# Kernel optimization log

Measured on AMD Instinct MI355X. Metric: run time of the kernel, lower is better.

The kernel has to match this reference:

```python
import jax, jax.numpy as jnp
import numpy as np

EPS = 1e-12  # TF l2_normalize epsilon


def setup_inputs() -> dict:
    key = jax.random.key(0)
    k1, k2 = jax.random.split(key)
    B, V, F = 32, 200000, 400000
    vertices = jax.random.normal(k1, (B, V, 3), dtype=jnp.float32)
    faces = jax.random.randint(k2, (F, 3), 0, V, dtype=jnp.int32)
    return {"vertices": vertices, "faces": faces}


def reference(vertices, faces):
    # vertices: [B, V, 3], faces: [F, 3]
    # Gather triangle vertices: [B, F, 3(verts), 3(xyz)]
    tri = vertices[:, faces, :]
    v0, v1, v2 = tri[..., 0, :], tri[..., 1, :], tri[..., 2, :]
    e1 = v0 - v1
    e2 = v2 - v1
    face_normals = jnp.cross(e2, e1)  # [B, F, 3], unnormalized
    # Scatter-add face normals onto each of the 3 face vertices
    vertex_normals = jnp.zeros_like(vertices)
    for i in range(3):
        vertex_normals = vertex_normals.at[:, faces[:, i], :].add(face_normals)
    # l2 normalize (TF semantics: x * rsqrt(max(sum(x^2), eps)))
    sq = jnp.sum(vertex_normals * vertex_normals, axis=-1, keepdims=True)
    vertex_normals = vertex_normals * jax.lax.rsqrt(jnp.maximum(sq, EPS))
    return vertex_normals
```

## Files before the change

### kernel.cpp

```cpp
#include <hip/hip_runtime.h>

#define EPS 1e-12f
#define CAP 32
#define CAPU 8

typedef unsigned long long ull;


__global__ void zero_ints(int* __restrict__ p, int n) {
    int i = blockIdx.x * blockDim.x + threadIdx.x;
    if (i < n) p[i] = 0;
}

__global__ __launch_bounds__(1024) void prep_kernel(const float* __restrict__ verts,
                                                    float* __restrict__ vT,
                                                    const int* __restrict__ faces,
                                                    int* __restrict__ cursor,
                                                    ull* __restrict__ ell,
                                                    int V, int fblk, int E) {
    __shared__ float sx[32][33], sy[32][33], sz[32][33];
    int bid = blockIdx.x;
    int q = bid / 6, r = bid - 6 * q;
    bool isfill = (r == 5) && (q < fblk);
    if (isfill) {
        int t = q * 1024 + threadIdx.x;
        if (t >= E) return;
        int f = t / 3;
        int c = t - 3 * f;
        int base = 3 * f;
        int iv = faces[base + c];
        int ia = faces[base + (c == 2 ? 0 : c + 1)];
        int ib = faces[base + (c == 0 ? 2 : c - 1)];
        int s = atomicAdd(&cursor[iv], 1);
        if (s < CAP) {
            ull e = ((ull)(unsigned)ib << 32) | (unsigned)ia;
            ell[(size_t)iv * CAP + s] = e;
        }
    } else {
        int t_id = bid - min(q + (r == 5 ? 1 : 0), fblk);
        int tx = threadIdx.x & 31, ty = threadIdx.x >> 5;
        int v0 = t_id * 32;
        const float* p = verts + ((size_t)ty * V + (v0 + tx)) * 3;
        sx[ty][tx] = __builtin_nontemporal_load(p + 0);
        sy[ty][tx] = __builtin_nontemporal_load(p + 1);
        sz[ty][tx] = __builtin_nontemporal_load(p + 2);
        __syncthreads();
        float* o = vT + (size_t)(v0 + ty) * 96;
        o[tx]      = sx[tx][ty];
        o[32 + tx] = sy[tx][ty];
        o[64 + tx] = sz[tx][ty];
    }
}

__global__ __launch_bounds__(1024) void gather_t(const float* __restrict__ vT,
                                                 const int* __restrict__ deg,
                                                 const ull* __restrict__ ell,
                                                 float* __restrict__ out,
                                                 int V) {
    __shared__ float sx[32][33], sy[32][33], sz[32][33];
    int b = threadIdx.x & 31;
    int vi = threadIdx.x >> 5;
    int v = blockIdx.x * 32 + vi;

    int d = min(__builtin_nontemporal_load(deg + v), CAP);
    const float* crow = vT + (size_t)v * 96;
    float vx = crow[b], vy = crow[32 + b], vz = crow[64 + b];
    const ull* ev = ell + (size_t)v * CAP;
    ull e[CAPU];
#pragma unroll
    for (int s = 0; s < CAPU; s++)
        e[s] = __builtin_nontemporal_load(ev + s);
    __builtin_amdgcn_sched_barrier(0);

    float Ax[CAPU], Ay[CAPU], Az[CAPU], Bx[CAPU], By[CAPU], Bz[CAPU];
#pragma unroll
    for (int s = 0; s < CAPU; s++) {
        unsigned ia = (s < d) ? (unsigned)(e[s] & 0xffffffffull) : 0u;
        unsigned ib = (s < d) ? (unsigned)(e[s] >> 32) : 0u;
        const float* ra = vT + (size_t)ia * 96;
        const float* rb = vT + (size_t)ib * 96;
        Ax[s] = ra[b]; Ay[s] = ra[32 + b]; Az[s] = ra[64 + b];
        Bx[s] = rb[b]; By[s] = rb[32 + b]; Bz[s] = rb[64 + b];
    }
    __builtin_amdgcn_sched_barrier(0);

    float ax = 0.f, ay = 0.f, az = 0.f;
#pragma unroll
    for (int s = 0; s < CAPU; s++) {
        if (s < d) {
            float aX = Ax[s] - vx, aY = Ay[s] - vy, aZ = Az[s] - vz;
            float bX = Bx[s] - vx, bY = By[s] - vy, bZ = Bz[s] - vz;
            ax += aY * bZ - aZ * bY;
            ay += aZ * bX - aX * bZ;
            az += aX * bY - aY * bX;
        }
    }
    for (int s = CAPU; s < d; s++) {
        ull cu = __builtin_nontemporal_load(ev + s);
        const float* ra = vT + (size_t)(unsigned)(cu & 0xffffffffull) * 96;
        const float* rb = vT + (size_t)(unsigned)(cu >> 32) * 96;
        float aX = ra[b] - vx, aY = ra[32 + b] - vy, aZ = ra[64 + b] - vz;
        float bX = rb[b] - vx, bY = rb[32 + b] - vy, bZ = rb[64 + b] - vz;
        ax += aY * bZ - aZ * bY;
        ay += aZ * bX - aX * bZ;
        az += aX * bY - aY * bX;
    }

    float scn = rsqrtf(fmaxf(ax * ax + ay * ay + az * az, EPS));
    sx[vi][b] = ax * scn; sy[vi][b] = ay * scn; sz[vi][b] = az * scn;
    __syncthreads();

    float* o = out + ((size_t)vi * V + (size_t)blockIdx.x * 32 + b) * 3;
    __builtin_nontemporal_store(sx[b][vi], o + 0);
    __builtin_nontemporal_store(sy[b][vi], o + 1);
    __builtin_nontemporal_store(sz[b][vi], o + 2);
}

extern "C" void kernel_launch(void* const* d_in, const int* in_sizes, int n_in,
                              void* d_out, int out_size, void* d_ws, size_t ws_size,
                              hipStream_t stream) {
    const float* verts = (const float*)d_in[0];
    const int* faces = (const int*)d_in[1];
    float* out = (float*)d_out;

    const int V = 200000;
    const int F = in_sizes[1] / 3;
    const int B = in_sizes[0] / (3 * V);
    const int E = 3 * F;
    (void)B;

    char* w = (char*)d_ws;
    float* vT = (float*)w;  w += (size_t)V * 96 * sizeof(float);
    int* cursor = (int*)w;  w += (size_t)V * sizeof(int);
    ull* ell = (ull*)w;

    zero_ints<<<(V + 255) / 256, 256, 0, stream>>>(cursor, V);

    int tblk = V / 32;
    int fblk = (E + 1023) / 1024;
    prep_kernel<<<tblk + fblk, 1024, 0, stream>>>(verts, vT, faces, cursor, ell,
                                                  V, fblk, E);

    gather_t<<<V / 32, 1024, 0, stream>>>(vT, cursor, ell, out, V);
}
```

Baseline: 353.2 us.

## Replace atomic cursor adjacency build with hashed CAS slots and ballot compaction

Drops the per-vertex degree counter and its zeroing kernel. Adjacency slots are now cleared to an EMPTY sentinel, interleaved with the vertex transpose, and filled by a separate kernel that claims slots with atomicCAS at hashed offsets. The gather kernel loads all 32 slots per vertex in one coalesced read and recovers degree and entry order with ballot, popcount and shuffles. In exchange it clears the whole 32-slot table (about 51 MB of stores) instead of 0.8 MB of counters, adds CAS retries on collisions, and splits the fill into a launch that no longer overlaps the transpose.

```diff
diff --git a/kernel.cpp b/kernel.cpp
--- a/kernel.cpp
+++ b/kernel.cpp
@@ -3,41 +3,26 @@
 #define EPS 1e-12f
 #define CAP 32
 #define CAPU 8
+#define EMPTY 0xFFFFFFFFFFFFFFFFull
 
 typedef unsigned long long ull;
 
 
-__global__ void zero_ints(int* __restrict__ p, int n) {
-    int i = blockIdx.x * blockDim.x + threadIdx.x;
-    if (i < n) p[i] = 0;
-}
-
-__global__ __launch_bounds__(1024) void prep_kernel(const float* __restrict__ verts,
-                                                    float* __restrict__ vT,
-                                                    const int* __restrict__ faces,
-                                                    int* __restrict__ cursor,
-                                                    ull* __restrict__ ell,
-                                                    int V, int fblk, int E) {
+__global__ __launch_bounds__(1024) void prep1(const float* __restrict__ verts,
+                                              float* __restrict__ vT,
+                                              ull* __restrict__ ellu,
+                                              int V, int nclr) {
     __shared__ float sx[32][33], sy[32][33], sz[32][33];
     int bid = blockIdx.x;
-    int q = bid / 6, r = bid - 6 * q;
-    bool isfill = (r == 5) && (q < fblk);
-    if (isfill) {
-        int t = q * 1024 + threadIdx.x;
-        if (t >= E) return;
-        int f = t / 3;
-        int c = t - 3 * f;
-        int base = 3 * f;
-        int iv = faces[base + c];
-        int ia = faces[base + (c == 2 ? 0 : c + 1)];
-        int ib = faces[base + (c == 0 ? 2 : c - 1)];
-        int s = atomicAdd(&cursor[iv], 1);
-        if (s < CAP) {
-            ull e = ((ull)(unsigned)ib << 32) | (unsigned)ia;
-            ell[(size_t)iv * CAP + s] = e;
+    int q = bid / 3, r = bid - 3 * q;
+    if (r == 2) {
+        int idx = q * 1024 + threadIdx.x;
+        if (idx < nclr) {
+            __builtin_nontemporal_store(EMPTY, ellu + 2 * (size_t)idx);
+            __builtin_nontemporal_store(EMPTY, ellu + 2 * (size_t)idx + 1);
         }
     } else {
-        int t_id = bid - min(q + (r == 5 ? 1 : 0), fblk);
+        int t_id = q * 2 + r;
         int tx = threadIdx.x & 31, ty = threadIdx.x >> 5;
         int v0 = t_id * 32;
         const float* p = verts + ((size_t)ty * V + (v0 + tx)) * 3;
@@ -52,8 +37,27 @@
     }
 }
 
+__global__ void fill_cas(const int* __restrict__ faces, ull* __restrict__ ell,
+                         int E) {
+    int t = blockIdx.x * blockDim.x + threadIdx.x;
+    if (t >= E) return;
+    int f = t / 3;
+    int c = t - 3 * f;
+    int base = 3 * f;
+    int iv = faces[base + c];
+    int ia = faces[base + (c == 2 ? 0 : c + 1)];
+    int ib = faces[base + (c == 0 ? 2 : c - 1)];
+    ull e = ((ull)(unsigned)ib << 32) | (unsigned)ia;
+    ull* bp = ell + (size_t)iv * CAP;
+    unsigned h = ((unsigned)t * 2654435761u) >> 27;
+#pragma unroll 4
+    for (int k = 0; k < CAP; k++) {
+        unsigned p = (h + k) & (CAP - 1);
+        if (atomicCAS(bp + p, EMPTY, e) == EMPTY) break;
+    }
+}
+
 __global__ __launch_bounds__(1024) void gather_t(const float* __restrict__ vT,
-                                                 const int* __restrict__ deg,
                                                  const ull* __restrict__ ell,
                                                  float* __restrict__ out,
                                                  int V) {
@@ -61,44 +65,60 @@
     int b = threadIdx.x & 31;
     int vi = threadIdx.x >> 5;
     int v = blockIdx.x * 32 + vi;
+    int half = (threadIdx.x & 63) >> 5;
 
-    int d = min(__builtin_nontemporal_load(deg + v), CAP);
+    ull eln = __builtin_nontemporal_load(ell + (size_t)v * CAP + b);
+    unsigned lo = (unsigned)eln, hi = (unsigned)(eln >> 32);
+    ull full = __ballot(eln != EMPTY);
+    unsigned mask = (unsigned)(full >> (half * 32));
+    int d = __popc(mask);
+
     const float* crow = vT + (size_t)v * 96;
     float vx = crow[b], vy = crow[32 + b], vz = crow[64 + b];
-    const ull* ev = ell + (size_t)v * CAP;
-    ull e[CAPU];
+
+    unsigned m = mask;
+    int ia[CAPU], ib[CAPU];
 #pragma unroll
-    for (int s = 0; s < CAPU; s++)
-        e[s] = __builtin_nontemporal_load(ev + s);
+    for (int j = 0; j < CAPU; j++) {
+        int l = m ? (__ffs(m) - 1) : 0;
+        m &= m - 1;
+        int src = half * 32 + l;
+        int lj = __shfl((int)lo, src);
+        int hj = __shfl((int)hi, src);
+        ia[j] = (j < d) ? lj : 0;
+        ib[j] = (j < d) ? hj : 0;
+    }
     __builtin_amdgcn_sched_barrier(0);
 
     float Ax[CAPU], Ay[CAPU], Az[CAPU], Bx[CAPU], By[CAPU], Bz[CAPU];
 #pragma unroll
-    for (int s = 0; s < CAPU; s++) {
-        unsigned ia = (s < d) ? (unsigned)(e[s] & 0xffffffffull) : 0u;
-        unsigned ib = (s < d) ? (unsigned)(e[s] >> 32) : 0u;
-        const float* ra = vT + (size_t)ia * 96;
-        const float* rb = vT + (size_t)ib * 96;
-        Ax[s] = ra[b]; Ay[s] = ra[32 + b]; Az[s] = ra[64 + b];
-        Bx[s] = rb[b]; By[s] = rb[32 + b]; Bz[s] = rb[64 + b];
+    for (int j = 0; j < CAPU; j++) {
+        const float* ra = vT + (size_t)(unsigned)ia[j] * 96;
+        const float* rb = vT + (size_t)(unsigned)ib[j] * 96;
+        Ax[j] = ra[b]; Ay[j] = ra[32 + b]; Az[j] = ra[64 + b];
+        Bx[j] = rb[b]; By[j] = rb[32 + b]; Bz[j] = rb[64 + b];
     }
     __builtin_amdgcn_sched_barrier(0);
 
     float ax = 0.f, ay = 0.f, az = 0.f;
 #pragma unroll
-    for (int s = 0; s < CAPU; s++) {
-        if (s < d) {
-            float aX = Ax[s] - vx, aY = Ay[s] - vy, aZ = Az[s] - vz;
-            float bX = Bx[s] - vx, bY = By[s] - vy, bZ = Bz[s] - vz;
+    for (int j = 0; j < CAPU; j++) {
+        if (j < d) {
+            float aX = Ax[j] - vx, aY = Ay[j] - vy, aZ = Az[j] - vz;
+            float bX = Bx[j] - vx, bY = By[j] - vy, bZ = Bz[j] - vz;
             ax += aY * bZ - aZ * bY;
             ay += aZ * bX - aX * bZ;
             az += aX * bY - aY * bX;
         }
     }
-    for (int s = CAPU; s < d; s++) {
-        ull cu = __builtin_nontemporal_load(ev + s);
-        const float* ra = vT + (size_t)(unsigned)(cu & 0xffffffffull) * 96;
-        const float* rb = vT + (size_t)(unsigned)(cu >> 32) * 96;
+    for (int j = CAPU; j < d; j++) {
+        int l = __ffs(m) - 1;
+        m &= m - 1;
+        int src = half * 32 + l;
+        int lj = __shfl((int)lo, src);
+        int hj = __shfl((int)hi, src);
+        const float* ra = vT + (size_t)(unsigned)lj * 96;
+        const float* rb = vT + (size_t)(unsigned)hj * 96;
         float aX = ra[b] - vx, aY = ra[32 + b] - vy, aZ = ra[64 + b] - vz;
         float bX = rb[b] - vx, bY = rb[32 + b] - vy, bZ = rb[64 + b] - vz;
         ax += aY * bZ - aZ * bY;
@@ -131,15 +151,14 @@
 
     char* w = (char*)d_ws;
     float* vT = (float*)w;  w += (size_t)V * 96 * sizeof(float);
-    int* cursor = (int*)w;  w += (size_t)V * sizeof(int);
     ull* ell = (ull*)w;
 
-    zero_ints<<<(V + 255) / 256, 256, 0, stream>>>(cursor, V);
+    int tblk = V / 32;
+    int nclr = (int)((size_t)V * CAP / 2);
+    int cblk = (nclr + 1023) / 1024;
+    prep1<<<tblk + cblk, 1024, 0, stream>>>(verts, vT, ell, V, nclr);
 
-    int tblk = V / 32;
-    int fblk = (E + 1023) / 1024;
-    prep_kernel<<<tblk + fblk, 1024, 0, stream>>>(verts, vT, faces, cursor, ell,
-                                                  V, fblk, E);
+    fill_cas<<<(E + 1023) / 1024, 1024, 0, stream>>>(faces, ell, E);
 
-    gather_t<<<V / 32, 1024, 0, stream>>>(vT, cursor, ell, out, V);
+    gather_t<<<V / 32, 1024, 0, stream>>>(vT, ell, out, V);
 }
```

Result: no change. 348.6 us (-1.3%).
